# Kernel optimization log

Measured on AMD Instinct MI355X. Metric: run time of the kernel, lower is better.

## Reference

```python
import jax, jax.numpy as jnp
import numpy as np

B, T, NA, NV, K, SD, H, E = 128, 64, 10, 16, 4, 512, 256, 32

def _lin(key, fan_in, fan_out):
    k1, k2 = jax.random.split(key)
    s = 1.0 / np.sqrt(fan_in)
    W = jax.random.uniform(k1, (fan_in, fan_out), jnp.float32, -s, s)
    b = jax.random.uniform(k2, (fan_out,), jnp.float32, -s, s)
    return W, b

def setup_inputs() -> dict:
    key = jax.random.key(0)
    ks = jax.random.split(key, 16)
    inp = {
        "qvals": jax.random.normal(ks[0], (B, T, NA), jnp.float32),
        "causal_relations": jax.random.randint(ks[1], (B, T, K, NV), 0, NA, jnp.int32),
        "states": jax.random.normal(ks[2], (B, T, SD), jnp.float32),
    }
    inp["w00_l1_W"], inp["w00_l1_b"] = _lin(ks[3], SD + NV, H)
    inp["w00_l2_W"], inp["w00_l2_b"] = _lin(ks[4], H, K)
    inp["b00_W"], inp["b00_b"] = _lin(ks[5], SD + NV, 1)
    inp["w01_W"], inp["w01_b"] = _lin(ks[6], SD, NA)
    inp["b01_W"], inp["b01_b"] = _lin(ks[7], SD, 1)
    inp["w1_l1_W"], inp["w1_l1_b"] = _lin(ks[8], SD, H)
    inp["w1_l2_W"], inp["w1_l2_b"] = _lin(ks[9], H, (NV + 1) * E)
    inp["b1_W"], inp["b1_b"] = _lin(ks[10], SD, E)
    inp["w2_l1_W"], inp["w2_l1_b"] = _lin(ks[11], SD, H)
    inp["w2_l2_W"], inp["w2_l2_b"] = _lin(ks[12], H, E)
    inp["b2_l1_W"], inp["b2_l1_b"] = _lin(ks[13], SD, E)
    inp["b2_l2_W"], inp["b2_l2_b"] = _lin(ks[14], E, 1)
    return inp

def reference(qvals, causal_relations, states,
              w00_l1_W, w00_l1_b, w00_l2_W, w00_l2_b, b00_W, b00_b,
              w01_W, w01_b, b01_W, b01_b,
              w1_l1_W, w1_l1_b, w1_l2_W, w1_l2_b, b1_W, b1_b,
              w2_l1_W, w2_l1_b, w2_l2_W, w2_l2_b,
              b2_l1_W, b2_l1_b, b2_l2_W, b2_l2_b):
    b, t, na = qvals.shape
    nv = causal_relations.shape[-1]
    sd = states.shape[-1]
    emb = b1_W.shape[1]

    # (b,t,k,nv) -> (b,t,nv,k); gather per-variable selected agent q-values
    cr = jnp.swapaxes(causal_relations, 2, 3)
    gathered = jnp.take_along_axis(qvals[:, :, None, :], cr, axis=-1)  # (b,t,nv,k)

    # Per-variable hypernets. Original builds a one-hot over n_variables but sets
    # var_onehot[variable] = 1, i.e. batch row `variable` becomes all-ones
    # (replicated faithfully). Split the first Linear into state part + onehot part:
    h_base = states @ w00_l1_W[:sd] + w00_l1_b   # (b,t,H)
    h_delta = w00_l1_W[sd:].sum(0)               # (H,)  contribution of all-ones onehot row
    g_base = states @ b00_W[:sd] + b00_b         # (b,t,1)
    g_delta = b00_W[sd:].sum(0)                  # (1,)

    def per_var(v):
        h = jax.nn.relu(h_base.at[v].add(h_delta))
        w0 = h @ w00_l2_W + w00_l2_b             # (b,t,k)
        b0 = g_base.at[v].add(g_delta)[..., 0]   # (b,t)
        return w0, b0

    w00, b00v = jax.vmap(per_var)(jnp.arange(nv))  # (nv,b,t,k), (nv,b,t)

    # group_qval_v = gathered_v @ |w0_v| + b0_v
    group = jnp.einsum('btvk,vbtk->btv', gathered, jnp.abs(w00)) + jnp.moveaxis(b00v, 0, -1)

    # residual agent mix (hyper_w0_1 / hyper_b0_1): plain linear hypernet, no abs in source
    w01 = states @ w01_W + w01_b                 # (b,t,na)
    other = jnp.einsum('bta,bta->bt', qvals, w01) + (states @ b01_W + b01_b)[..., 0]
    gq = jnp.concatenate([group, other[..., None]], axis=-1)  # (b,t,nv+1)

    # QMIX-style two-layer mix with hypernet weights
    w1 = jnp.abs((jax.nn.relu(states @ w1_l1_W + w1_l1_b) @ w1_l2_W + w1_l2_b)
                 .reshape(b, t, nv + 1, emb))
    b1 = states @ b1_W + b1_b                    # (b,t,E)
    hidden = jax.nn.elu(jnp.einsum('btv,btve->bte', gq, w1) + b1)
    w2 = jnp.abs(jax.nn.relu(states @ w2_l1_W + w2_l1_b) @ w2_l2_W + w2_l2_b)  # (b,t,E)
    b2 = jax.nn.relu(states @ b2_l1_W + b2_l1_b) @ b2_l2_W + b2_l2_b           # (b,t,1)
    y = jnp.sum(hidden * w2, axis=-1, keepdims=True) + b2
    return y  # (b,t,1)
```

## Files before the change

kernel.cpp:

```cpp
#include <hip/hip_runtime.h>
#include <hip/hip_bf16.h>


typedef __hip_bfloat16 bf16;
typedef unsigned short ushort_t;
typedef __attribute__((ext_vector_type(8))) short short8;
typedef __attribute__((ext_vector_type(4))) float f32x4;

#define PA_OFF 0
#define PA_TILES 56
#define PB_OFF (PA_TILES * 16 * 64 * 8 * 2)
#define PB_TILES 36
#define FB_OFF (PB_OFF + PB_TILES * 8 * 64 * 8 * 2)
#define NCST 2854
#define WS_NEED (size_t)(FB_OFF + NCST * 4 + 32)

#define MFMA16(a, b, c) __builtin_amdgcn_mfma_f32_16x16x32_bf16(a, b, c, 0, 0, 0)

__device__ __forceinline__ float us2f(ushort_t x) {
  unsigned u = ((unsigned)x) << 16; float f; __builtin_memcpy(&f, &u, 4); return f;
}
__device__ __forceinline__ ushort_t f2us(float v) {
  bf16 h = __float2bfloat16(v); ushort_t r; __builtin_memcpy(&r, &h, 2); return r;
}
template <bool F32>
__device__ __forceinline__ float LD(const void* p, size_t i) {
  if (F32) return ((const float*)p)[i];
  return us2f(((const ushort_t*)p)[i]);
}

__device__ __forceinline__ int detect_f32(const void* states) {
  const unsigned short* u = (const unsigned short*)states;
  int lane = threadIdx.x & 63;
  int bad = 0;
  for (int i = lane; i < 512; i += 64) {
    unsigned short x = u[i];
    int e = (x >> 7) & 0xFF;
    if (e > 140 || (((x & 0x7FFFu) != 0) && e < 100)) bad++;
  }
  for (int off = 32; off; off >>= 1) bad += __shfl_down(bad, off);
  return __shfl(bad, 0) > 20;
}

__device__ __forceinline__ void pa_store(ushort_t* pa, int np, int k, ushort_t v) {
  int t = np >> 4, lm = np & 15, ks = k >> 5, qq = (k >> 3) & 3, j = k & 7;
  pa[(size_t)t * 8192 + ks * 512 + (qq * 16 + lm) * 8 + j] = v;
}
__device__ __forceinline__ void pb_store(ushort_t* pb, int np, int k, ushort_t v) {
  int t = np >> 4, lm = np & 15, ks = k >> 5, qq = (k >> 3) & 3, j = k & 7;
  pb[(size_t)t * 4096 + ks * 512 + (qq * 16 + lm) * 8 + j] = v;
}

template <bool F32>
__device__ void prep_body(int gtid, int T, char* ws,
    const void* w00l1W, const void* w00l1b, const void* w00l2W, const void* w00l2b,
    const void* b00W, const void* b00b,
    const void* w01W, const void* w01b, const void* b01W, const void* b01b,
    const void* w1l1W, const void* w1l1b, const void* w1l2W, const void* w1l2b,
    const void* b1W, const void* b1b,
    const void* w2l1W, const void* w2l1b, const void* w2l2W, const void* w2l2b,
    const void* b2l1W, const void* b2l1b, const void* b2l2W, const void* b2l2b) {
  ushort_t* pa = (ushort_t*)(ws + PA_OFF);
  ushort_t* pb = (ushort_t*)(ws + PB_OFF);
  float* cst = (float*)(ws + FB_OFF);
  for (int i = gtid; i < 131072; i += T) {
    int k = i >> 8, n = i & 255;
    pa_store(pa, n, k, f2us(LD<F32>(w1l1W, i)));
    pa_store(pa, 256 + n, k, f2us(LD<F32>(w2l1W, i)));
    pa_store(pa, 512 + n, k, f2us(LD<F32>(w00l1W, i)));
  }
  for (int i = gtid; i < 16384; i += T) {
    int k = i >> 5, n = i & 31;
    pa_store(pa, 768 + n, k, f2us(LD<F32>(b1W, i)));
    pa_store(pa, 800 + n, k, f2us(LD<F32>(b2l1W, i)));
  }
  for (int i = gtid; i < 5120; i += T) {
    int k = i / 10, n = i % 10;
    pa_store(pa, 832 + n, k, f2us(LD<F32>(w01W, i)));
  }
  for (int i = gtid; i < 512; i += T) {
    pa_store(pa, 842, i, f2us(LD<F32>(b00W, i)));
    pa_store(pa, 843, i, f2us(LD<F32>(b01W, i)));
  }
  for (int z = gtid; z < 2048; z += T) {
    int ks = z >> 7, qq = (z >> 5) & 3, lm = 12 + ((z >> 3) & 3), j = z & 7;
    pa[(size_t)52 * 8192 + ks * 512 + (qq * 16 + lm) * 8 + j] = 0;
  }
  for (int i = gtid; i < 139264; i += T) {
    int k = i / 544, n = i % 544;
    pb_store(pb, n, k, f2us(LD<F32>(w1l2W, i)));
  }
  for (int i = gtid; i < 8192; i += T) {
    int k = i >> 5, n = i & 31;
    pb_store(pb, 544 + n, k, f2us(LD<F32>(w2l2W, i)));
  }
  for (int i = gtid; i < NCST; i += T) {
    float x;
    if (i < 896) {
      int c = i;
      if (c < 256) x = LD<F32>(w1l1b, c);
      else if (c < 512) x = LD<F32>(w2l1b, c - 256);
      else if (c < 768) x = LD<F32>(w00l1b, c - 512);
      else if (c < 800) x = LD<F32>(b1b, c - 768);
      else if (c < 832) x = LD<F32>(b2l1b, c - 800);
      else if (c < 842) x = LD<F32>(w01b, c - 832);
      else if (c == 842) x = LD<F32>(b00b, 0);
      else if (c == 843) x = LD<F32>(b01b, 0);
      else x = 0.f;
    } else if (i < 1536) {
      int c = i - 896;
      x = (c < 544) ? LD<F32>(w1l2b, c) : (c < 576 ? LD<F32>(w2l2b, c - 544) : 0.f);
    } else if (i < 1792) {
      int j = i - 1536; float s = 0.f;
      for (int z = 0; z < 16; ++z) s += LD<F32>(w00l1W, (size_t)(512 + z) * 256 + j);
      x = s;
    } else if (i < 2816) x = LD<F32>(w00l2W, i - 1792);
    else if (i < 2820) x = LD<F32>(w00l2b, i - 2816);
    else if (i < 2852) x = LD<F32>(b2l2W, i - 2820);
    else if (i == 2852) x = LD<F32>(b2l2b, 0);
    else { float s = 0.f; for (int z = 0; z < 16; ++z) s += LD<F32>(b00W, 512 + z); x = s; }
    cst[i] = x;
  }
}

__global__ __launch_bounds__(256) void prep_kernel(char* ws, const void* states,
    const void* w00l1W, const void* w00l1b, const void* w00l2W, const void* w00l2b,
    const void* b00W, const void* b00b,
    const void* w01W, const void* w01b, const void* b01W, const void* b01b,
    const void* w1l1W, const void* w1l1b, const void* w1l2W, const void* w1l2b,
    const void* b1W, const void* b1b,
    const void* w2l1W, const void* w2l1b, const void* w2l2W, const void* w2l2b,
    const void* b2l1W, const void* b2l1b, const void* b2l2W, const void* b2l2b) {
  int gtid = blockIdx.x * 256 + threadIdx.x;
  int T = gridDim.x * 256;
  if (detect_f32(states))
    prep_body<true>(gtid, T, ws, w00l1W, w00l1b, w00l2W, w00l2b, b00W, b00b,
        w01W, w01b, b01W, b01b, w1l1W, w1l1b, w1l2W, w1l2b, b1W, b1b,
        w2l1W, w2l1b, w2l2W, w2l2b, b2l1W, b2l1b, b2l2W, b2l2b);
  else
    prep_body<false>(gtid, T, ws, w00l1W, w00l1b, w00l2W, w00l2b, b00W, b00b,
        w01W, w01b, b01W, b01b, w1l1W, w1l1b, w1l2W, w1l2b, b1W, b1b,
        w2l1W, w2l1b, w2l2W, w2l2b, b2l1W, b2l1b, b2l2W, b2l2b);
}

struct SmemM {
  union {
    __align__(16) ushort_t sA[2][8192];
    __align__(16) ushort_t w1a[32][544];
  } u;
  __align__(16) ushort_t Am1[2][4096];
  __align__(16) ushort_t Am2[2][4096];
  __align__(16) ushort_t hb[32][264];
  float hd[256];
  float b1v[32][32];
  float rbv[32][32];
  float w2v[32][32];
  float w01v[32][12];
  float qv[32][10];
  unsigned char cr[32][64];
  float w0c[32][4], w0s[32][4];
  float gq[32][18];
  float gbv[32], b01v[32];
  float hid[32][33];
};

template <bool F32>
__device__ void mixer_body(SmemM& sm, const char* ws, int n0,
    const void* qvals, const int* crel, const void* states, void* out) {
  const int tid = threadIdx.x;
  const int lane = tid & 63, wv = tid >> 6;
  const int q = lane >> 4, lm = lane & 15;
  const int b_blk = n0 >> 6;
  const ushort_t* pa = (const ushort_t*)(ws + PA_OFF);
  const ushort_t* pb = (const ushort_t*)(ws + PB_OFF);
  const float* cstg = (const float*)(ws + FB_OFF);

  for (int fi = tid; fi < 2048; fi += 512) {
    int ln = fi & 63, ks = (fi >> 6) & 15, G = fi >> 10;
    int row = G * 16 + (ln & 15), col = ks * 32 + (ln >> 4) * 8;
    if (F32) {
      const f32x4* p = (const f32x4*)((const float*)states + (size_t)(n0 + row) * 512 + col);
      f32x4 v0 = p[0], v1 = p[1];
      ushort_t v[8];
      v[0] = f2us(v0[0]); v[1] = f2us(v0[1]); v[2] = f2us(v0[2]); v[3] = f2us(v0[3]);
      v[4] = f2us(v1[0]); v[5] = f2us(v1[1]); v[6] = f2us(v1[2]); v[7] = f2us(v1[3]);
      *(short8*)&sm.u.sA[G][(size_t)(ks * 64 + ln) * 8] = *(short8*)v;
    } else {
      *(short8*)&sm.u.sA[G][(size_t)(ks * 64 + ln) * 8] =
          *(const short8*)((const ushort_t*)states + (size_t)(n0 + row) * 512 + col);
    }
  }
  for (int i = tid; i < 320; i += 512) sm.qv[i / 10][i % 10] = LD<F32>(qvals, (size_t)(n0 + i / 10) * 10 + i % 10);
  for (int i = tid; i < 2048; i += 512) sm.cr[i >> 6][i & 63] = (unsigned char)crel[(size_t)n0 * 64 + i];
  if (tid < 256) sm.hd[tid] = cstg[1536 + tid];
  __syncthreads();

  short8 nb[16];
  {
    const ushort_t* bp = pa + (size_t)wv * 8192 + lane * 8;
#pragma unroll
    for (int ks = 0; ks < 16; ++ks) nb[ks] = *(const short8*)(bp + ks * 512);
  }
  for (int s = wv; s < 53; s += 8) {
    short8 cb[16];
#pragma unroll
    for (int ks = 0; ks < 16; ++ks) cb[ks] = nb[ks];
    if (s + 8 < 53) {
      const ushort_t* bp = pa + (size_t)(s + 8) * 8192 + lane * 8;
#pragma unroll
      for (int ks = 0; ks < 16; ++ks) nb[ks] = *(const short8*)(bp + ks * 512);
    }
    f32x4 acc0 = {0.f, 0.f, 0.f, 0.f}, acc1 = {0.f, 0.f, 0.f, 0.f};
#pragma unroll
    for (int ks = 0; ks < 16; ++ks) {
      short8 a0 = *(const short8*)&sm.u.sA[0][(ks * 64 + lane) * 8];
      short8 a1 = *(const short8*)&sm.u.sA[1][(ks * 64 + lane) * 8];
      acc0 = MFMA16(a0, cb[ks], acc0);
      acc1 = MFMA16(a1, cb[ks], acc1);
    }
    int c = s * 16 + lm;
    if (c < 844) {
      float bias = cstg[c];
      int ks2 = (c & 255) >> 5, q2 = (c >> 3) & 3, j2 = c & 7;
#pragma unroll
      for (int G = 0; G < 2; ++G) {
        f32x4 acc = G ? acc1 : acc0;
        int rb = G * 16 + q * 4;
        if (c < 256) {
#pragma unroll
          for (int g = 0; g < 4; ++g) {
            float v = acc[g] + bias;
            sm.Am1[G][(ks2 * 64 + q2 * 16 + q * 4 + g) * 8 + j2] = f2us(v > 0.f ? v : 0.f);
          }
        } else if (c < 512) {
#pragma unroll
          for (int g = 0; g < 4; ++g) {
            float v = acc[g] + bias;
            sm.Am2[G][(ks2 * 64 + q2 * 16 + q * 4 + g) * 8 + j2] = f2us(v > 0.f ? v : 0.f);
          }
        } else if (c < 768) {
#pragma unroll
          for (int g = 0; g < 4; ++g) sm.hb[rb + g][c - 512] = f2us(acc[g] + bias);
        } else if (c < 800) {
#pragma unroll
          for (int g = 0; g < 4; ++g) sm.b1v[rb + g][c - 768] = acc[g] + bias;
        } else if (c < 832) {
#pragma unroll
          for (int g = 0; g < 4; ++g) { float v = acc[g] + bias; sm.rbv[rb + g][c - 800] = v > 0.f ? v : 0.f; }
        } else if (c < 842) {
#pragma unroll
          for (int g = 0; g < 4; ++g) sm.w01v[rb + g][c - 832] = acc[g] + bias;
        } else if (c == 842) {
#pragma unroll
          for (int g = 0; g < 4; ++g) sm.gbv[rb + g] = acc[g] + bias;
        } else {
#pragma unroll
          for (int g = 0; g < 4; ++g) sm.b01v[rb + g] = acc[g] + bias;
        }
      }
    }
  }
  __syncthreads();

  short8 nb2[8];
  {
    const ushort_t* bp = pb + (size_t)wv * 4096 + lane * 8;
#pragma unroll
    for (int ks = 0; ks < 8; ++ks) nb2[ks] = *(const short8*)(bp + ks * 512);
  }
  for (int t = wv; t < 36; t += 8) {
    short8 cb2[8];
#pragma unroll
    for (int ks = 0; ks < 8; ++ks) cb2[ks] = nb2[ks];
    if (t + 8 < 36) {
      const ushort_t* bp = pb + (size_t)(t + 8) * 4096 + lane * 8;
#pragma unroll
      for (int ks = 0; ks < 8; ++ks) nb2[ks] = *(const short8*)(bp + ks * 512);
    }
    const ushort_t* A0 = (t < 34) ? sm.Am1[0] : sm.Am2[0];
    const ushort_t* A1 = (t < 34) ? sm.Am1[1] : sm.Am2[1];
    f32x4 c0 = {0.f, 0.f, 0.f, 0.f}, c1 = {0.f, 0.f, 0.f, 0.f};
#pragma unroll
    for (int ks = 0; ks < 8; ++ks) {
      short8 x0 = *(const short8*)(A0 + (ks * 64 + lane) * 8);
      short8 x1 = *(const short8*)(A1 + (ks * 64 + lane) * 8);
      c0 = MFMA16(x0, cb2[ks], c0);
      c1 = MFMA16(x1, cb2[ks], c1);
    }
    int c = t * 16 + lm;
    float bias = cstg[896 + c];
#pragma unroll
    for (int G = 0; G < 2; ++G) {
      f32x4 acc = G ? c1 : c0;
      int rb = G * 16 + q * 4;
      if (c < 544) {
#pragma unroll
        for (int g = 0; g < 4; ++g) sm.u.w1a[rb + g][c] = f2us(fabsf(acc[g] + bias));
      } else {
        int e = c - 544;
#pragma unroll
        for (int g = 0; g < 4; ++g) sm.w2v[rb + g][e] = fabsf(acc[g] + bias);
      }
    }
  }
  __syncthreads();

  if (tid < 256) {
    int r = tid >> 3, k = (tid >> 1) & 3, sflag = tid & 1;
    const float* wl = cstg + 1792;
    float a = 0.f;
    for (int j = 0; j < 256; ++j) {
      float h = us2f(sm.hb[r][j]);
      if (sflag) h += sm.hd[j];
      h = h > 0.f ? h : 0.f;
      a = fmaf(h, wl[j * 4 + k], a);
    }
    a += cstg[2816 + k];
    if (sflag) sm.w0s[r][k] = a; else sm.w0c[r][k] = a;
  }
  __syncthreads();

  {
    int r = tid >> 4, v = tid & 15;
    bool sp = (v == b_blk);
    const float* w0 = sp ? sm.w0s[r] : sm.w0c[r];
    float g = sm.gbv[r] + (sp ? cstg[2853] : 0.f);
#pragma unroll
    for (int k = 0; k < 4; ++k) {
      int a = sm.cr[r][k * 16 + v];
      g = fmaf(sm.qv[r][a], fabsf(w0[k]), g);
    }
    sm.gq[r][v] = g;
  }
  if (tid < 32) {
    float o = sm.b01v[tid];
#pragma unroll
    for (int a = 0; a < 10; ++a) o = fmaf(sm.qv[tid][a], sm.w01v[tid][a], o);
    sm.gq[tid][16] = o;
  }
  __syncthreads();

  for (int p = tid; p < 1024; p += 512) {
    int r = p >> 5, e = p & 31;
    float h = sm.b1v[r][e];
#pragma unroll
    for (int v = 0; v < 17; ++v) h = fmaf(sm.gq[r][v], us2f(sm.u.w1a[r][v * 32 + e]), h);
    float hid = h > 0.f ? h : (expf(h) - 1.f);
    sm.hid[r][e] = hid * sm.w2v[r][e] + sm.rbv[r][e] * cstg[2820 + e];
  }
  __syncthreads();

  if (tid < 32) {
    float y = cstg[2852];
#pragma unroll
    for (int e = 0; e < 32; ++e) y += sm.hid[tid][e];
    if (F32) ((float*)out)[n0 + tid] = y;
    else ((bf16*)out)[n0 + tid] = __float2bfloat16(y);
  }
}

__global__ __launch_bounds__(512, 2) void causal_mixer_mfma(const char* ws,
    const void* qvals, const int* crel, const void* states, void* out) {
  __shared__ SmemM sm;
  int n0 = blockIdx.x * 32;
  if (detect_f32(states))
    mixer_body<true>(sm, ws, n0, qvals, crel, states, out);
  else
    mixer_body<false>(sm, ws, n0, qvals, crel, states, out);
}

struct SmemF {
  float s[16][516]; float buf[16][258]; float hd[256];
  float q[16][10]; int cr[16][66];
  float w0c[16][4], w0s[16][4]; float gq[16][17];
  float w01[16][10]; float b01[16]; float gb[16]; float gd;
  float hid[16][32]; float w2[16][32]; float rb[16][32];
};

template <bool F32>
__device__ void fb_body(SmemF& sm, int tid, int n0, int b_blk,
    const void* qvals, const int* crel, const void* states,
    const void* w00l1W, const void* w00l1b, const void* w00l2W, const void* w00l2b,
    const void* b00W, const void* b00b,
    const void* w01W, const void* w01b, const void* b01W, const void* b01b,
    const void* w1l1W, const void* w1l1b, const void* w1l2W, const void* w1l2b,
    const void* b1W, const void* b1b,
    const void* w2l1W, const void* w2l1b, const void* w2l2W, const void* w2l2b,
    const void* b2l1W, const void* b2l1b, const void* b2l2W, const void* b2l2b,
    void* out) {
  for (int idx = tid; idx < 16 * 512; idx += 256) {
    int r = idx >> 9, i = idx & 511;
    sm.s[r][i] = LD<F32>(states, (size_t)(n0 + r) * 512 + i);
  }
  for (int idx = tid; idx < 160; idx += 256) {
    int r = idx / 10, a = idx % 10;
    sm.q[r][a] = LD<F32>(qvals, (size_t)(n0 + r) * 10 + a);
  }
  for (int idx = tid; idx < 16 * 64; idx += 256) {
    int r = idx >> 6, kv = idx & 63;
    sm.cr[r][kv] = crel[(size_t)(n0 + r) * 64 + kv];
  }
  if (tid == 0) {
    float gd = 0.f;
    for (int i = 512; i < 528; ++i) gd += LD<F32>(b00W, i);
    sm.gd = gd;
  }
  __syncthreads();
  {
    const int j = tid;
    float hd = 0.f;
    for (int i = 0; i < 16; ++i) hd += LD<F32>(w00l1W, (size_t)(512 + i) * 256 + j);
    sm.hd[j] = hd;
    float acc[16]; float bj = LD<F32>(w00l1b, j);
#pragma unroll
    for (int r = 0; r < 16; ++r) acc[r] = bj;
    for (int i = 0; i < 512; ++i) {
      float w = LD<F32>(w00l1W, (size_t)i * 256 + j);
#pragma unroll
      for (int r = 0; r < 16; ++r) acc[r] = fmaf(sm.s[r][i], w, acc[r]);
    }
#pragma unroll
    for (int r = 0; r < 16; ++r) sm.buf[r][j] = acc[r];
  }
  __syncthreads();
  if (tid < 64) {
    int r = tid >> 2, k = tid & 3;
    float aC = 0.f, aS = 0.f;
    for (int j = 0; j < 256; ++j) {
      float hb = sm.buf[r][j];
      float w = LD<F32>(w00l2W, j * 4 + k);
      float hc = hb > 0.f ? hb : 0.f;
      float hbs = hb + sm.hd[j];
      float hsv = hbs > 0.f ? hbs : 0.f;
      aC = fmaf(hc, w, aC); aS = fmaf(hsv, w, aS);
    }
    float bk = LD<F32>(w00l2b, k);
    sm.w0c[r][k] = aC + bk; sm.w0s[r][k] = aS + bk;
  } else if (tid < 224) {
    int p = tid - 64; int r = p / 10, a = p % 10;
    float acc = 0.f;
    for (int i = 0; i < 512; ++i) acc = fmaf(sm.s[r][i], LD<F32>(w01W, (size_t)i * 10 + a), acc);
    sm.w01[r][a] = acc + LD<F32>(w01b, a);
  } else if (tid < 240) {
    int r = tid - 224;
    float acc = 0.f;
    for (int i = 0; i < 512; ++i) acc = fmaf(sm.s[r][i], LD<F32>(b00W, i), acc);
    sm.gb[r] = acc + LD<F32>(b00b, 0);
  } else {
    int r = tid - 240;
    float acc = 0.f;
    for (int i = 0; i < 512; ++i) acc = fmaf(sm.s[r][i], LD<F32>(b01W, i), acc);
    sm.b01[r] = acc + LD<F32>(b01b, 0);
  }
  __syncthreads();
  {
    int r = tid >> 4, v = tid & 15;
    bool sp = (v == b_blk);
    const float* w0 = sp ? sm.w0s[r] : sm.w0c[r];
    float g = sm.gb[r] + (sp ? sm.gd : 0.f);
#pragma unroll
    for (int k = 0; k < 4; ++k) {
      int a = sm.cr[r][k * 16 + v];
      g = fmaf(sm.q[r][a], fabsf(w0[k]), g);
    }
    sm.gq[r][v] = g;
  }
  if (tid < 16) {
    int r = tid;
    float o = sm.b01[r];
    for (int a = 0; a < 10; ++a) o = fmaf(sm.q[r][a], sm.w01[r][a], o);
    sm.gq[r][16] = o;
  }
  __syncthreads();
  {
    const int j = tid;
    float acc[16]; float bj = LD<F32>(w1l1b, j);
#pragma unroll
    for (int r = 0; r < 16; ++r) acc[r] = bj;
    for (int i = 0; i < 512; ++i) {
      float w = LD<F32>(w1l1W, (size_t)i * 256 + j);
#pragma unroll
      for (int r = 0; r < 16; ++r) acc[r] = fmaf(sm.s[r][i], w, acc[r]);
    }
#pragma unroll
    for (int r = 0; r < 16; ++r) sm.buf[r][j] = acc[r] > 0.f ? acc[r] : 0.f;
  }
  __syncthreads();
  for (int p = tid; p < 512; p += 256) {
    int r = p >> 5, e = p & 31;
    float acc = 0.f;
    for (int v = 0; v < 17; ++v) {
      int c = v * 32 + e;
      float d = LD<F32>(w1l2b, c);
      for (int j = 0; j < 256; ++j) d = fmaf(sm.buf[r][j], LD<F32>(w1l2W, (size_t)j * 544 + c), d);
      acc = fmaf(sm.gq[r][v], fabsf(d), acc);
    }
    float b1v = LD<F32>(b1b, e);
    for (int i = 0; i < 512; ++i) b1v = fmaf(sm.s[r][i], LD<F32>(b1W, (size_t)i * 32 + e), b1v);
    float x = acc + b1v;
    sm.hid[r][e] = x > 0.f ? x : (expf(x) - 1.f);
  }
  __syncthreads();
  {
    const int j = tid;
    float acc[16]; float bj = LD<F32>(w2l1b, j);
#pragma unroll
    for (int r = 0; r < 16; ++r) acc[r] = bj;
    for (int i = 0; i < 512; ++i) {
      float w = LD<F32>(w2l1W, (size_t)i * 256 + j);
#pragma unroll
      for (int r = 0; r < 16; ++r) acc[r] = fmaf(sm.s[r][i], w, acc[r]);
    }
#pragma unroll
    for (int r = 0; r < 16; ++r) sm.buf[r][j] = acc[r] > 0.f ? acc[r] : 0.f;
  }
  __syncthreads();
  for (int p = tid; p < 512; p += 256) {
    int r = p >> 5, e = p & 31;
    float d = LD<F32>(w2l2b, e);
    for (int j = 0; j < 256; ++j) d = fmaf(sm.buf[r][j], LD<F32>(w2l2W, (size_t)j * 32 + e), d);
    sm.w2[r][e] = fabsf(d);
    float rb = LD<F32>(b2l1b, e);
    for (int i = 0; i < 512; ++i) rb = fmaf(sm.s[r][i], LD<F32>(b2l1W, (size_t)i * 32 + e), rb);
    sm.rb[r][e] = rb > 0.f ? rb : 0.f;
  }
  __syncthreads();
  if (tid < 16) {
    int r = tid;
    float y = 0.f;
#pragma unroll
    for (int e = 0; e < 32; ++e) y = fmaf(sm.hid[r][e], sm.w2[r][e], y);
    float b2v = LD<F32>(b2l2b, 0);
#pragma unroll
    for (int e = 0; e < 32; ++e) b2v = fmaf(sm.rb[r][e], LD<F32>(b2l2W, e), b2v);
    float yv = y + b2v;
    if (F32) ((float*)out)[n0 + r] = yv;
    else ((bf16*)out)[n0 + r] = __float2bfloat16(yv);
  }
}

__global__ __launch_bounds__(256) void causal_mixer_fb(
    const void* qvals, const int* crel, const void* states,
    const void* w00l1W, const void* w00l1b, const void* w00l2W, const void* w00l2b,
    const void* b00W, const void* b00b,
    const void* w01W, const void* w01b, const void* b01W, const void* b01b,
    const void* w1l1W, const void* w1l1b, const void* w1l2W, const void* w1l2b,
    const void* b1W, const void* b1b,
    const void* w2l1W, const void* w2l1b, const void* w2l2W, const void* w2l2b,
    const void* b2l1W, const void* b2l1b, const void* b2l2W, const void* b2l2b,
    void* out) {
  __shared__ SmemF sm;
  const int tid = threadIdx.x;
  const int n0 = blockIdx.x * 16;
  const int b_blk = n0 >> 6;
  if (detect_f32(states))
    fb_body<true>(sm, tid, n0, b_blk, qvals, crel, states, w00l1W, w00l1b, w00l2W, w00l2b,
        b00W, b00b, w01W, w01b, b01W, b01b, w1l1W, w1l1b, w1l2W, w1l2b, b1W, b1b,
        w2l1W, w2l1b, w2l2W, w2l2b, b2l1W, b2l1b, b2l2W, b2l2b, out);
  else
    fb_body<false>(sm, tid, n0, b_blk, qvals, crel, states, w00l1W, w00l1b, w00l2W, w00l2b,
        b00W, b00b, w01W, w01b, b01W, b01b, w1l1W, w1l1b, w1l2W, w1l2b, b1W, b1b,
        w2l1W, w2l1b, w2l2W, w2l2b, b2l1W, b2l1b, b2l2W, b2l2b, out);
}

extern "C" void kernel_launch(void* const* d_in, const int* in_sizes, int n_in,
                              void* d_out, int out_size, void* d_ws, size_t ws_size,
                              hipStream_t stream) {
  char* ws = (char*)d_ws;
  if (ws_size >= WS_NEED) {
    hipLaunchKernelGGL(prep_kernel, dim3(256), dim3(256), 0, stream, ws, d_in[2],
        d_in[3], d_in[4], d_in[5], d_in[6], d_in[7], d_in[8],
        d_in[9], d_in[10], d_in[11], d_in[12],
        d_in[13], d_in[14], d_in[15], d_in[16], d_in[17], d_in[18],
        d_in[19], d_in[20], d_in[21], d_in[22], d_in[23], d_in[24],
        d_in[25], d_in[26]);
    hipLaunchKernelGGL(causal_mixer_mfma, dim3(256), dim3(512), 0, stream, ws,
        d_in[0], (const int*)d_in[1], d_in[2], d_out);
  } else {
    hipLaunchKernelGGL(causal_mixer_fb, dim3(512), dim3(256), 0, stream,
        d_in[0], (const int*)d_in[1], d_in[2],
        d_in[3], d_in[4], d_in[5], d_in[6], d_in[7], d_in[8],
        d_in[9], d_in[10], d_in[11], d_in[12],
        d_in[13], d_in[14], d_in[15], d_in[16], d_in[17], d_in[18],
        d_in[19], d_in[20], d_in[21], d_in[22], d_in[23], d_in[24],
        d_in[25], d_in[26],
        d_out);
  }
}
```

Before: 167.8 us.

## Interchange MFMA GEMM loops to reuse A fragments across all column tiles

Both hypernet GEMM phases now make each wave hold accumulators for all of its column tiles (7 and 5) at once and iterate over k-steps in the outer loop. Each A fragment is read from LDS once per k-step instead of once per tile, and the B loads for the next k-step are issued one step ahead. The cost is many more live accumulator registers (up to 28 VGPRs of f32x4 state per group) and redundant MFMAs on padded tiles for waves with fewer real tiles, which may lower occupancy.

```diff
diff --git a/kernel.cpp b/kernel.cpp
--- a/kernel.cpp
+++ b/kernel.cpp
@@ -195,36 +195,48 @@
   if (tid < 256) sm.hd[tid] = cstg[1536 + tid];
   __syncthreads();
 
-  short8 nb[16];
   {
-    const ushort_t* bp = pa + (size_t)wv * 8192 + lane * 8;
-#pragma unroll
-    for (int ks = 0; ks < 16; ++ks) nb[ks] = *(const short8*)(bp + ks * 512);
-  }
-  for (int s = wv; s < 53; s += 8) {
-    short8 cb[16];
-#pragma unroll
-    for (int ks = 0; ks < 16; ++ks) cb[ks] = nb[ks];
-    if (s + 8 < 53) {
-      const ushort_t* bp = pa + (size_t)(s + 8) * 8192 + lane * 8;
-#pragma unroll
-      for (int ks = 0; ks < 16; ++ks) nb[ks] = *(const short8*)(bp + ks * 512);
-    }
-    f32x4 acc0 = {0.f, 0.f, 0.f, 0.f}, acc1 = {0.f, 0.f, 0.f, 0.f};
+    int sidx[7]; bool sreal[7];
+#pragma unroll
+    for (int i = 0; i < 7; ++i) {
+      int s = wv + 8 * i;
+      sreal[i] = (s < 53);
+      sidx[i] = sreal[i] ? s : wv;
+    }
+    f32x4 accA[7][2];
+#pragma unroll
+    for (int i = 0; i < 7; ++i) { accA[i][0] = (f32x4){0,0,0,0}; accA[i][1] = (f32x4){0,0,0,0}; }
+    const ushort_t* base = pa + lane * 8;
+    short8 cur[7], nxt[7];
+#pragma unroll
+    for (int i = 0; i < 7; ++i) cur[i] = *(const short8*)(base + (size_t)sidx[i] * 8192);
 #pragma unroll
     for (int ks = 0; ks < 16; ++ks) {
+      if (ks < 15) {
+#pragma unroll
+        for (int i = 0; i < 7; ++i)
+          nxt[i] = *(const short8*)(base + (size_t)sidx[i] * 8192 + (ks + 1) * 512);
+      }
       short8 a0 = *(const short8*)&sm.u.sA[0][(ks * 64 + lane) * 8];
       short8 a1 = *(const short8*)&sm.u.sA[1][(ks * 64 + lane) * 8];
-      acc0 = MFMA16(a0, cb[ks], acc0);
-      acc1 = MFMA16(a1, cb[ks], acc1);
-    }
-    int c = s * 16 + lm;
-    if (c < 844) {
+#pragma unroll
+      for (int i = 0; i < 7; ++i) {
+        accA[i][0] = MFMA16(a0, cur[i], accA[i][0]);
+        accA[i][1] = MFMA16(a1, cur[i], accA[i][1]);
+      }
+#pragma unroll
+      for (int i = 0; i < 7; ++i) cur[i] = nxt[i];
+    }
+#pragma unroll
+    for (int i = 0; i < 7; ++i) {
+      if (!sreal[i]) continue;
+      int c = sidx[i] * 16 + lm;
+      if (c >= 844) continue;
       float bias = cstg[c];
       int ks2 = (c & 255) >> 5, q2 = (c >> 3) & 3, j2 = c & 7;
 #pragma unroll
       for (int G = 0; G < 2; ++G) {
-        f32x4 acc = G ? acc1 : acc0;
+        f32x4 acc = accA[i][G];
         int rb = G * 16 + q * 4;
         if (c < 256) {
 #pragma unroll
@@ -262,44 +274,59 @@
   }
   __syncthreads();
 
-  short8 nb2[8];
   {
-    const ushort_t* bp = pb + (size_t)wv * 4096 + lane * 8;
-#pragma unroll
-    for (int ks = 0; ks < 8; ++ks) nb2[ks] = *(const short8*)(bp + ks * 512);
-  }
-  for (int t = wv; t < 36; t += 8) {
-    short8 cb2[8];
-#pragma unroll
-    for (int ks = 0; ks < 8; ++ks) cb2[ks] = nb2[ks];
-    if (t + 8 < 36) {
-      const ushort_t* bp = pb + (size_t)(t + 8) * 4096 + lane * 8;
-#pragma unroll
-      for (int ks = 0; ks < 8; ++ks) nb2[ks] = *(const short8*)(bp + ks * 512);
-    }
-    const ushort_t* A0 = (t < 34) ? sm.Am1[0] : sm.Am2[0];
-    const ushort_t* A1 = (t < 34) ? sm.Am1[1] : sm.Am2[1];
-    f32x4 c0 = {0.f, 0.f, 0.f, 0.f}, c1 = {0.f, 0.f, 0.f, 0.f};
+    int tix[5]; bool treal[5];
+#pragma unroll
+    for (int i = 0; i < 5; ++i) {
+      int t = wv + 8 * i;
+      treal[i] = (t < 36);
+      tix[i] = treal[i] ? t : wv;
+    }
+    f32x4 accB[5][2];
+#pragma unroll
+    for (int i = 0; i < 5; ++i) { accB[i][0] = (f32x4){0,0,0,0}; accB[i][1] = (f32x4){0,0,0,0}; }
+    const ushort_t* base = pb + lane * 8;
+    short8 cur[5], nxt[5];
+#pragma unroll
+    for (int i = 0; i < 5; ++i) cur[i] = *(const short8*)(base + (size_t)tix[i] * 4096);
 #pragma unroll
     for (int ks = 0; ks < 8; ++ks) {
-      short8 x0 = *(const short8*)(A0 + (ks * 64 + lane) * 8);
-      short8 x1 = *(const short8*)(A1 + (ks * 64 + lane) * 8);
-      c0 = MFMA16(x0, cb2[ks], c0);
-      c1 = MFMA16(x1, cb2[ks], c1);
-    }
-    int c = t * 16 + lm;
-    float bias = cstg[896 + c];
-#pragma unroll
-    for (int G = 0; G < 2; ++G) {
-      f32x4 acc = G ? c1 : c0;
-      int rb = G * 16 + q * 4;
-      if (c < 544) {
-#pragma unroll
-        for (int g = 0; g < 4; ++g) sm.u.w1a[rb + g][c] = f2us(fabsf(acc[g] + bias));
-      } else {
-        int e = c - 544;
-#pragma unroll
-        for (int g = 0; g < 4; ++g) sm.w2v[rb + g][e] = fabsf(acc[g] + bias);
+      if (ks < 7) {
+#pragma unroll
+        for (int i = 0; i < 5; ++i)
+          nxt[i] = *(const short8*)(base + (size_t)tix[i] * 4096 + (ks + 1) * 512);
+      }
+      short8 m1a0 = *(const short8*)&sm.Am1[0][(ks * 64 + lane) * 8];
+      short8 m1a1 = *(const short8*)&sm.Am1[1][(ks * 64 + lane) * 8];
+      short8 m2a0 = *(const short8*)&sm.Am2[0][(ks * 64 + lane) * 8];
+      short8 m2a1 = *(const short8*)&sm.Am2[1][(ks * 64 + lane) * 8];
+#pragma unroll
+      for (int i = 0; i < 5; ++i) {
+        short8 x0 = (tix[i] < 34) ? m1a0 : m2a0;
+        short8 x1 = (tix[i] < 34) ? m1a1 : m2a1;
+        accB[i][0] = MFMA16(x0, cur[i], accB[i][0]);
+        accB[i][1] = MFMA16(x1, cur[i], accB[i][1]);
+      }
+#pragma unroll
+      for (int i = 0; i < 5; ++i) cur[i] = nxt[i];
+    }
+#pragma unroll
+    for (int i = 0; i < 5; ++i) {
+      if (!treal[i]) continue;
+      int c = tix[i] * 16 + lm;
+      float bias = cstg[896 + c];
+#pragma unroll
+      for (int G = 0; G < 2; ++G) {
+        f32x4 acc = accB[i][G];
+        int rb = G * 16 + q * 4;
+        if (c < 544) {
+#pragma unroll
+          for (int g = 0; g < 4; ++g) sm.u.w1a[rb + g][c] = f2us(fabsf(acc[g] + bias));
+        } else {
+          int e = c - 544;
+#pragma unroll
+          for (int g = 0; g < 4; ++g) sm.w2v[rb + g][e] = fabsf(acc[g] + bias);
+        }
       }
     }
   }
```

After: 170.5 us. About the same (+1.6%).
